# Optimization experiments

Measured on AMD Instinct MI355X. Metric: run time of the kernel, lower is better.

The kernel has to match this reference:

```python
import jax, jax.numpy as jnp
import numpy as np

N = 100000
H = 8      # heads
C = 8      # out channels per head
NEG_SLOPE = 0.2
EPS = 1e-16


def setup_inputs() -> dict:
    key = jax.random.key(0)
    k1, k2, k3, k4, k5, k6 = jax.random.split(key, 6)
    x = jax.random.normal(k1, (N, 128), dtype=jnp.float32)
    edge_index = jax.random.randint(k2, (2, 1600000), 0, N, dtype=jnp.int64)
    W = jax.random.normal(k3, (128, H * C), dtype=jnp.float32) * (1.0 / np.sqrt(128))
    att_src = jax.random.normal(k4, (H, C), dtype=jnp.float32)
    att_dst = jax.random.normal(k5, (H, C), dtype=jnp.float32)
    bias = jax.random.normal(k6, (H * C,), dtype=jnp.float32) * 0.01
    return {"x": x, "edge_index": edge_index, "W": W,
            "att_src": att_src, "att_dst": att_dst, "bias": bias}


def _gat_forward(x, edge_index, W, att_src, att_dst, bias):
    # add self loops (PyG GATConv default add_self_loops=True)
    loop = jnp.arange(N, dtype=edge_index.dtype)
    src = jnp.concatenate([edge_index[0], loop])
    dst = jnp.concatenate([edge_index[1], loop])

    h = (x @ W).reshape(N, H, C)                       # [N,H,C]
    a_src = jnp.sum(h * att_src, axis=-1)              # [N,H]
    a_dst = jnp.sum(h * att_dst, axis=-1)              # [N,H]

    e = a_src[src] + a_dst[dst]                        # [E,H]
    e = jnp.where(e > 0, e, NEG_SLOPE * e)             # leaky_relu(0.2)

    # segment softmax over edges grouped by destination node
    m = jax.ops.segment_max(e, dst, num_segments=N)    # [N,H]
    m = jnp.where(jnp.isfinite(m), m, 0.0)
    ex = jnp.exp(e - m[dst])                           # [E,H]
    denom = jax.ops.segment_sum(ex, dst, num_segments=N)
    alpha = ex / (denom[dst] + EPS)                    # [E,H]

    msg = alpha[:, :, None] * h[src]                   # [E,H,C]
    out = jax.ops.segment_sum(msg, dst, num_segments=N)  # [N,H,C]
    out = out.reshape(N, H * C) + bias
    return jax.nn.relu(out)


def reference(x, edge_index, W, att_src, att_dst, bias):
    return _gat_forward(x, edge_index, W, att_src, att_dst, bias)
```

## Files before the change

### kernel.cpp

```cpp
#include <hip/hip_runtime.h>
#include <hip/hip_bf16.h>

#define NNODES 100000
#define NH 8
#define OUTD 64
#define FDIM 128
#define NEG_SLOPE 0.2f
#define NBUCK ((NNODES + 255) / 256)
#define MAXB 5376
#define CH 4096
#define ROWS_PB 128
#define NFB ((NNODES + ROWS_PB - 1) / ROWS_PB)
#define SHST 68

typedef __attribute__((ext_vector_type(8))) short bf16x8;
typedef __attribute__((ext_vector_type(4))) float f32x4;
typedef __attribute__((ext_vector_type(4))) unsigned int u32x4;

static __device__ __forceinline__ unsigned short f2bf(float f) {
    __hip_bfloat16 b = __float2bfloat16(f);
    return *(unsigned short*)&b;
}

__global__ void k_wprep(const float* __restrict__ W, unsigned short* __restrict__ wimg)
{
    int i = blockIdx.x * 256 + threadIdx.x;
    if (i >= FDIM * OUTD) return;
    int k = i >> 6, col = i & 63;
    int chs = (k >> 3) ^ (col & 15);
    wimg[col * FDIM + chs * 8 + (k & 7)] = f2bf(W[i]);
}

__global__ __launch_bounds__(256) void k_feat(
    const float* __restrict__ x, const unsigned short* __restrict__ wimg,
    const float* __restrict__ att_s, const float* __restrict__ att_d,
    __hip_bfloat16* __restrict__ h, float* __restrict__ asrc,
    float* __restrict__ adst)
{
    __shared__ unsigned short sx[ROWS_PB * FDIM];
    __shared__ unsigned short swt[OUTD * FDIM];
    __shared__ float shf[4 * 16 * SHST];
    __shared__ float sAs[OUTD], sAd[OUTD];

    int tid = threadIdx.x;
    if (tid < OUTD) { sAs[tid] = att_s[tid]; sAd[tid] = att_d[tid]; }

    {
        const u32x4* src = (const u32x4*)wimg;
        u32x4* dst = (u32x4*)swt;
        for (int i = tid; i < (OUTD * FDIM) / 8; i += 256) dst[i] = src[i];
    }
    int row0 = blockIdx.x * ROWS_PB;
    for (int c = tid; c < ROWS_PB * 16; c += 256) {
        int row = c >> 4, chunk = c & 15;
        int grow = row0 + row;
        unsigned short tmp[8];
        if (grow < NNODES) {
            const float* p = x + (size_t)grow * FDIM + chunk * 8;
            f32x4 f0 = *(const f32x4*)p;
            f32x4 f1 = *(const f32x4*)(p + 4);
#pragma unroll
            for (int j = 0; j < 4; ++j) tmp[j] = f2bf(f0[j]);
#pragma unroll
            for (int j = 0; j < 4; ++j) tmp[4 + j] = f2bf(f1[j]);
        } else {
#pragma unroll
            for (int j = 0; j < 8; ++j) tmp[j] = 0;
        }
        int chs = chunk ^ (row & 15);
        *(bf16x8*)&sx[row * FDIM + chs * 8] = *(bf16x8*)tmp;
    }
    __syncthreads();

    int w = tid >> 6, l = tid & 63;
    int l4 = l & 15, g = l >> 4;

    bf16x8 bfrag[16];
#pragma unroll
    for (int n = 0; n < 4; ++n)
#pragma unroll
        for (int kk = 0; kk < 4; ++kk) {
            int col = n * 16 + l4;
            int chs = (kk * 4 + g) ^ l4;
            bfrag[n * 4 + kk] = *(const bf16x8*)&swt[col * FDIM + chs * 8];
        }

    float* mysh = &shf[w * 16 * SHST];

#pragma unroll
    for (int rt = 0; rt < 2; ++rt) {
        int lbase = w * 32 + rt * 16;
        f32x4 acc[4];
#pragma unroll
        for (int n = 0; n < 4; ++n) acc[n] = (f32x4){0.f, 0.f, 0.f, 0.f};

#pragma unroll
        for (int kk = 0; kk < 4; ++kk) {
            int row = lbase + l4;
            int chs = (kk * 4 + g) ^ l4;
            bf16x8 a = *(const bf16x8*)&sx[row * FDIM + chs * 8];
#pragma unroll
            for (int n = 0; n < 4; ++n)
                acc[n] = __builtin_amdgcn_mfma_f32_16x16x32_bf16(
                    a, bfrag[n * 4 + kk], acc[n], 0, 0, 0);
        }

#pragma unroll
        for (int n = 0; n < 4; ++n)
#pragma unroll
            for (int r = 0; r < 4; ++r)
                mysh[(g * 4 + r) * SHST + n * 16 + l4] = acc[n][r];

#pragma unroll
        for (int i = 0; i < 2; ++i) {
            int c = i * 64 + l;
            int row = c >> 3, ch = c & 7;
            int grow = row0 + lbase + row;
            if (grow < NNODES) {
                const float* rp = &mysh[row * SHST + ch * 8];
                unsigned short tmp[8];
#pragma unroll
                for (int j = 0; j < 8; ++j) tmp[j] = f2bf(rp[j]);
                *(bf16x8*)&h[(size_t)grow * OUTD + ch * 8] = *(bf16x8*)tmp;
            }
        }
#pragma unroll
        for (int i = 0; i < 2; ++i) {
            int t = i * 64 + l;
            int row = t >> 3, hd = t & 7;
            int grow = row0 + lbase + row;
            if (grow < NNODES) {
                const float* rp = &mysh[row * SHST + hd * 8];
                float s1 = 0.f, s2 = 0.f;
#pragma unroll
                for (int j = 0; j < 8; ++j) {
                    s1 = fmaf(rp[j], sAs[hd * 8 + j], s1);
                    s2 = fmaf(rp[j], sAd[hd * 8 + j], s2);
                }
                asrc[grow * NH + hd] = s1;
                adst[grow * NH + hd] = s2;
            }
        }
    }
}

__global__ __launch_bounds__(256) void k_bin(
    const int* __restrict__ ei, int E, int* __restrict__ gCur,
    unsigned int* __restrict__ gSorted)
{
    __shared__ int cnt[NBUCK];
    __shared__ int base[NBUCK];
    int tot = E + NNODES;
    int e0 = blockIdx.x * CH;
    int e1 = e0 + CH; if (e1 > tot) e1 = tot;

    for (int i = threadIdx.x; i < NBUCK; i += 256) cnt[i] = 0;
    __syncthreads();

    for (int i = e0 + threadIdx.x; i < e1; i += 256) {
        int d = (i < E) ? ei[E + i] : (i - E);
        atomicAdd(&cnt[d >> 8], 1);
    }
    __syncthreads();

    for (int i = threadIdx.x; i < NBUCK; i += 256) {
        int c = cnt[i];
        base[i] = (c > 0) ? atomicAdd(&gCur[i], c) : 0;
        cnt[i] = 0;
    }
    __syncthreads();

    for (int i = e0 + threadIdx.x; i < e1; i += 256) {
        int s, d;
        if (i < E) { s = ei[i]; d = ei[E + i]; }
        else       { s = d = i - E; }
        int b = d >> 8;
        int p = base[b] + atomicAdd(&cnt[b], 1);
        if (p < MAXB)
            gSorted[(size_t)b * MAXB + p] =
                ((unsigned int)(d & 255) << 17) | (unsigned int)s;
    }
}

__global__ __launch_bounds__(256) void k_csr(
    const int* __restrict__ gCur, unsigned int* __restrict__ gSorted,
    int2* __restrict__ rows)
{
    __shared__ unsigned int ent[MAXB];
    __shared__ int cnt[256], scn[256], cur[256];
    int b = blockIdx.x;
    int n = gCur[b]; if (n > MAXB) n = MAXB;
    size_t gbase = (size_t)b * MAXB;

    for (int i = threadIdx.x; i < n; i += 256) ent[i] = gSorted[gbase + i];
    cnt[threadIdx.x] = 0;
    __syncthreads();

    for (int i = threadIdx.x; i < n; i += 256)
        atomicAdd(&cnt[ent[i] >> 17], 1);
    __syncthreads();

    int v = cnt[threadIdx.x];
    int acc = v;
    scn[threadIdx.x] = v;
    __syncthreads();
    for (int off = 1; off < 256; off <<= 1) {
        int t = (threadIdx.x >= (unsigned)off) ? scn[threadIdx.x - off] : 0;
        __syncthreads();
        acc += t;
        scn[threadIdx.x] = acc;
        __syncthreads();
    }
    int ex = acc - v;

    int node = (b << 8) + threadIdx.x;
    if (node < NNODES)
        rows[node] = make_int2((int)gbase + ex, (int)gbase + ex + v);
    cur[threadIdx.x] = ex;
    __syncthreads();

    for (int i = threadIdx.x; i < n; i += 256) {
        unsigned int p = ent[i];
        int pos = atomicAdd(&cur[p >> 17], 1);
        gSorted[gbase + pos] = p & 0x1FFFFu;
    }
}

__global__ __launch_bounds__(256) void k_gather(
    const int2* __restrict__ rows, const unsigned int* __restrict__ esrc,
    const __hip_bfloat16* __restrict__ h, const float* __restrict__ asrc,
    const float* __restrict__ adst, const float* __restrict__ bias,
    float* __restrict__ out)
{
    int node = (blockIdx.x * 256 + threadIdx.x) >> 6;
    if (node >= NNODES) return;
    int lane = threadIdx.x & 63;
    int l5 = lane >> 5;
    int c  = lane & 31;
    int hh = c >> 2;

    float adh = adst[(unsigned)(node * NH + hh)];
    int2 se = rows[node];
    int start = se.x, end = se.y;
    const unsigned* hu = (const unsigned*)h;

    float num0 = 0.f, num1 = 0.f, den = 0.f;

    for (int base = start; base < end; base += 64) {
        int cnt = end - base; if (cnt > 64) cnt = 64;
        int sj = (base + lane < end) ? (int)esrc[base + lane] : 0;

        auto pair = [&](int k) {
            int s2 = __shfl(sj, k + l5);
            float a = asrc[(unsigned)(s2 * NH + hh)];
            unsigned w = hu[(unsigned)(s2 * 32 + c)];
            float e = a + adh;
            e = fmaxf(e, NEG_SLOPE * e);
            float ex = __expf(e);
            den += ex;
            union { unsigned u; float f; } lo, hi;
            lo.u = w << 16; hi.u = w & 0xffff0000u;
            num0 = fmaf(ex, lo.f, num0);
            num1 = fmaf(ex, hi.f, num1);
        };

        int k = 0;
        for (; k + 4 <= cnt; k += 4) { pair(k); pair(k + 2); }
        for (; k + 2 <= cnt; k += 2) { pair(k); }
        if (k < cnt) {
            int s2 = __shfl(sj, k);
            float a = asrc[(unsigned)(s2 * NH + hh)];
            unsigned w = hu[(unsigned)(s2 * 32 + c)];
            float e = a + adh;
            e = fmaxf(e, NEG_SLOPE * e);
            float ex = l5 ? 0.f : __expf(e);
            den += ex;
            union { unsigned u; float f; } lo, hi;
            lo.u = w << 16; hi.u = w & 0xffff0000u;
            num0 = fmaf(ex, lo.f, num0);
            num1 = fmaf(ex, hi.f, num1);
        }
    }

    num0 += __shfl_xor(num0, 32);
    num1 += __shfl_xor(num1, 32);
    den  += __shfl_xor(den, 32);

    int ch = c * 2 + l5;
    float inv = 1.f / (den + 1e-16f);
    float vv = (l5 ? num1 : num0) * inv + bias[ch];
    out[(unsigned)(node * OUTD + ch)] = vv > 0.f ? vv : 0.f;
}

extern "C" void kernel_launch(void* const* d_in, const int* in_sizes, int n_in,
                              void* d_out, int out_size, void* d_ws, size_t ws_size,
                              hipStream_t stream)
{
    const float* x     = (const float*)d_in[0];
    const int*   ei    = (const int*)  d_in[1];
    const float* W     = (const float*)d_in[2];
    const float* att_s = (const float*)d_in[3];
    const float* att_d = (const float*)d_in[4];
    const float* bias  = (const float*)d_in[5];
    float* out = (float*)d_out;
    int E = in_sizes[1] / 2;
    int tot = E + NNODES;

    __hip_bfloat16* h = (__hip_bfloat16*)d_ws;
    float* asrc   = (float*)(h + (size_t)NNODES * OUTD);
    float* adst   = asrc + (size_t)NNODES * NH;
    int2*  rows   = (int2*)(adst + (size_t)NNODES * NH);
    int*   gCur   = (int*)(rows + NNODES);
    unsigned int* gSorted = (unsigned int*)(gCur + 512);
    unsigned short* wimg  = (unsigned short*)(gSorted + (size_t)NBUCK * MAXB);

    hipMemsetAsync(gCur, 0, 512 * sizeof(int), stream);

    k_wprep<<<(FDIM * OUTD + 255) / 256, 256, 0, stream>>>(W, wimg);
    k_feat<<<NFB, 256, 0, stream>>>(x, wimg, att_s, att_d, h, asrc, adst);
    k_bin<<<(tot + CH - 1) / CH, 256, 0, stream>>>(ei, E, gCur, gSorted);
    k_csr<<<NBUCK, 256, 0, stream>>>(gCur, gSorted, rows);
    k_gather<<<(NNODES * 64 + 255) / 256, 256, 0, stream>>>(
        rows, gSorted, h, asrc, adst, bias, out);
}
```

Measured before the change: 125.4 us.

## Batch gather loads across four edge pairs, warp-shuffle CSR scan, larger chunk

The gather loop now issues the index shuffles and all asrc/h loads for four edge pairs (eight edges) before doing any exp/FMA work, so more independent memory requests are in flight per wave. The CSR kernel's block-wide Hillis-Steele scan, which used shared memory and many __syncthreads, is replaced by a wavefront shuffle scan plus a small per-wave offset sum. The edge bucketing chunk size CH is doubled. These add register pressure in the gather kernel, and larger chunks mean fewer, longer blocks in the bucketing step.

```diff
diff --git a/kernel.cpp b/kernel.cpp
--- a/kernel.cpp
+++ b/kernel.cpp
@@ -8,7 +8,7 @@
 #define NEG_SLOPE 0.2f
 #define NBUCK ((NNODES + 255) / 256)
 #define MAXB 5376
-#define CH 4096
+#define CH 8192
 #define ROWS_PB 128
 #define NFB ((NNODES + ROWS_PB - 1) / ROWS_PB)
 #define SHST 68
@@ -187,39 +187,43 @@
     int2* __restrict__ rows)
 {
     __shared__ unsigned int ent[MAXB];
-    __shared__ int cnt[256], scn[256], cur[256];
+    __shared__ int cnt[256], cur[256];
+    __shared__ int wsum[4];
     int b = blockIdx.x;
     int n = gCur[b]; if (n > MAXB) n = MAXB;
     size_t gbase = (size_t)b * MAXB;
-
-    for (int i = threadIdx.x; i < n; i += 256) ent[i] = gSorted[gbase + i];
-    cnt[threadIdx.x] = 0;
-    __syncthreads();
-
-    for (int i = threadIdx.x; i < n; i += 256)
+    int tid = threadIdx.x;
+
+    for (int i = tid; i < n; i += 256) ent[i] = gSorted[gbase + i];
+    cnt[tid] = 0;
+    __syncthreads();
+
+    for (int i = tid; i < n; i += 256)
         atomicAdd(&cnt[ent[i] >> 17], 1);
     __syncthreads();
 
-    int v = cnt[threadIdx.x];
+    int v = cnt[tid];
+    int lane = tid & 63, wid = tid >> 6;
     int acc = v;
-    scn[threadIdx.x] = v;
-    __syncthreads();
-    for (int off = 1; off < 256; off <<= 1) {
-        int t = (threadIdx.x >= (unsigned)off) ? scn[threadIdx.x - off] : 0;
-        __syncthreads();
-        acc += t;
-        scn[threadIdx.x] = acc;
-        __syncthreads();
-    }
-    int ex = acc - v;
-
-    int node = (b << 8) + threadIdx.x;
+#pragma unroll
+    for (int off = 1; off < 64; off <<= 1) {
+        int t = __shfl_up(acc, off);
+        if (lane >= off) acc += t;
+    }
+    if (lane == 63) wsum[wid] = acc;
+    __syncthreads();
+    int woff = 0;
+#pragma unroll
+    for (int i = 0; i < 4; ++i) woff += (i < wid) ? wsum[i] : 0;
+    int ex = acc + woff - v;
+
+    int node = (b << 8) + tid;
     if (node < NNODES)
         rows[node] = make_int2((int)gbase + ex, (int)gbase + ex + v);
-    cur[threadIdx.x] = ex;
-    __syncthreads();
-
-    for (int i = threadIdx.x; i < n; i += 256) {
+    cur[tid] = ex;
+    __syncthreads();
+
+    for (int i = tid; i < n; i += 256) {
         unsigned int p = ent[i];
         int pos = atomicAdd(&cur[p >> 17], 1);
         gSorted[gbase + pos] = p & 0x1FFFFu;
@@ -265,7 +269,34 @@
         };
 
         int k = 0;
-        for (; k + 4 <= cnt; k += 4) { pair(k); pair(k + 2); }
+        for (; k + 8 <= cnt; k += 8) {
+            int sA = __shfl(sj, k + 0 + l5);
+            int sB = __shfl(sj, k + 2 + l5);
+            int sC = __shfl(sj, k + 4 + l5);
+            int sD = __shfl(sj, k + 6 + l5);
+            float aA = asrc[(unsigned)(sA * NH + hh)];
+            float aB = asrc[(unsigned)(sB * NH + hh)];
+            float aC = asrc[(unsigned)(sC * NH + hh)];
+            float aD = asrc[(unsigned)(sD * NH + hh)];
+            unsigned wA = hu[(unsigned)(sA * 32 + c)];
+            unsigned wB = hu[(unsigned)(sB * 32 + c)];
+            unsigned wC = hu[(unsigned)(sC * 32 + c)];
+            unsigned wD = hu[(unsigned)(sD * 32 + c)];
+            float eA = aA + adh; eA = fmaxf(eA, NEG_SLOPE * eA); eA = __expf(eA);
+            float eB = aB + adh; eB = fmaxf(eB, NEG_SLOPE * eB); eB = __expf(eB);
+            float eC = aC + adh; eC = fmaxf(eC, NEG_SLOPE * eC); eC = __expf(eC);
+            float eD = aD + adh; eD = fmaxf(eD, NEG_SLOPE * eD); eD = __expf(eD);
+            den += eA; den += eB; den += eC; den += eD;
+            union { unsigned u; float f; } lo, hi;
+            lo.u = wA << 16; hi.u = wA & 0xffff0000u;
+            num0 = fmaf(eA, lo.f, num0); num1 = fmaf(eA, hi.f, num1);
+            lo.u = wB << 16; hi.u = wB & 0xffff0000u;
+            num0 = fmaf(eB, lo.f, num0); num1 = fmaf(eB, hi.f, num1);
+            lo.u = wC << 16; hi.u = wC & 0xffff0000u;
+            num0 = fmaf(eC, lo.f, num0); num1 = fmaf(eC, hi.f, num1);
+            lo.u = wD << 16; hi.u = wD & 0xffff0000u;
+            num0 = fmaf(eD, lo.f, num0); num1 = fmaf(eD, hi.f, num1);
+        }
         for (; k + 2 <= cnt; k += 2) { pair(k); }
         if (k < cnt) {
             int s2 = __shfl(sj, k);
```

Result: no change. 124.9 us (-0.4%).
